# Kernel tuning notes

Hardware: AMD Instinct MI355X
Metric: run time of the kernel (lower is better)

## Reference

```python
import jax, jax.numpy as jnp
import numpy as np

B, S, D = 4, 4096, 1024
DECAY = 0.95


def setup_inputs() -> dict:
    key = jax.random.key(0)
    ks = jax.random.split(key, 7)
    sc = 1.0 / np.sqrt(D)
    return {
        "h": jax.random.normal(ks[0], (B, S, D), jnp.float32),
        "chunk_size": 128,
        "Wq": jax.random.normal(ks[1], (D, D), jnp.float32) * sc,
        "Wk": jax.random.normal(ks[2], (D, D), jnp.float32) * sc,
        "Wv": jax.random.normal(ks[3], (D, D), jnp.float32) * sc,
        "Wo": jax.random.normal(ks[4], (D, D), jnp.float32) * sc,
        "Wg": jax.random.normal(ks[5], (D, D), jnp.float32) * sc,
        "bg": jnp.zeros((D,), jnp.float32),
    }


def reference(h, chunk_size, Wq, Wk, Wv, Wo, Wg, bg):
    bsz, seq_len, d_model = h.shape
    n_chunks = seq_len // chunk_size  # S divisible by chunk_size

    # projections (torch nn.Linear: y = x @ W.T)
    q = jnp.einsum('bsd,ed->bse', h, Wq)
    k = jnp.einsum('bsd,ed->bse', h, Wk)
    v = jnp.einsum('bsd,ed->bse', h, Wv)
    gate = jax.nn.sigmoid(jnp.einsum('bsd,ed->bse', h, Wg) + bg)

    def to_chunks(x):  # [B,S,D] -> [n_chunks, B, T, D]
        return x.reshape(bsz, n_chunks, chunk_size, d_model).transpose(1, 0, 2, 3)

    qc, kc, vc, gc = map(to_chunks, (q, k, v, gate))

    def step(state, inp):
        q_c, k_c, v_c, g_c = inp
        kv = jnp.einsum('btd,bte->bde', k_c, v_c) / chunk_size
        state = DECAY * state + (1.0 - DECAY) * kv
        ret = jnp.einsum('btd,bde->bte', q_c, state)
        return state, ret * g_c

    state0 = jnp.zeros((bsz, d_model, d_model), h.dtype)
    _, out_chunks = jax.lax.scan(step, state0, (qc, kc, vc, gc))
    out = out_chunks.transpose(1, 0, 2, 3).reshape(bsz, seq_len, d_model)
    return jnp.einsum('bsd,ed->bse', out, Wo)
```

## Files before the change

### kernel.cpp

```cpp
#include <hip/hip_runtime.h>
#include <math.h>

#define B_ 4
#define S_ 4096
#define D_ 1024
#define T_ 128
#define NC_ 32
#define DECAY_ 0.95f
#define NPAIR_ 528

typedef __bf16 bf16;
typedef __bf16 bf16x8 __attribute__((ext_vector_type(8)));
typedef __bf16 bf16x4 __attribute__((ext_vector_type(4)));
typedef float f32x4 __attribute__((ext_vector_type(4)));

__device__ __forceinline__ f32x4 mfma16(bf16x8 a, bf16x8 b, f32x4 c) {
  return __builtin_amdgcn_mfma_f32_16x16x32_bf16(a, b, c, 0, 0, 0);
}

__device__ __forceinline__ void gload16(const bf16* g, bf16* l) {
  __builtin_amdgcn_global_load_lds(
      (const __attribute__((address_space(1))) unsigned int*)g,
      (__attribute__((address_space(3))) unsigned int*)l, 16, 0, 0);
}

__global__ void cast_kernel(const float* __restrict__ src, bf16* __restrict__ dst, int n) {
  int i = (blockIdx.x * blockDim.x + threadIdx.x) * 4;
  int stride = gridDim.x * blockDim.x * 4;
  for (; i < n; i += stride) {
    float4 f = *(const float4*)(src + i);
    bf16x4 o = { (bf16)f.x, (bf16)f.y, (bf16)f.z, (bf16)f.w };
    *(bf16x4*)(dst + i) = o;
  }
}

__global__ void wcast_kernel(const float* __restrict__ Wq, const float* __restrict__ Wk,
                             const float* __restrict__ Wv, const float* __restrict__ Wg,
                             const float* __restrict__ Wo,
                             bf16* __restrict__ Wcat, bf16* __restrict__ Wo_bf) {
  const int NW = 1 << 20;
  long gid = ((long)blockIdx.x * blockDim.x + threadIdx.x) * 4;
  int sel = (int)(gid >> 20);
  int off = (int)(gid & (NW - 1));
  const float* src = (sel == 0) ? Wq : (sel == 1) ? Wk : (sel == 2) ? Wv
                   : (sel == 3) ? Wg : Wo;
  bf16* dst = (sel < 4) ? (Wcat + (long)sel * NW) : Wo_bf;
  float4 f = *(const float4*)(src + off);
  bf16x4 o = { (bf16)f.x, (bf16)f.y, (bf16)f.z, (bf16)f.w };
  *(bf16x4*)(dst + off) = o;
}

__global__ __launch_bounds__(256) void gemm_proj(
    const bf16* __restrict__ A, const bf16* __restrict__ W,
    const float* __restrict__ bg,
    bf16* __restrict__ qo, bf16* __restrict__ ko,
    bf16* __restrict__ vT, bf16* __restrict__ go)
{
  __shared__ __align__(16) bf16 As[128 * 64];
  __shared__ __align__(16) bf16 Bs[128 * 64];
  const int K = 1024;
  int m0 = blockIdx.y * 128;
  int n0 = blockIdx.x * 128;
  int tid = threadIdx.x;
  int l = tid & 63, w = tid >> 6;
  int wr = w >> 1, wc = w & 1;
  int wbase = w << 9;

  const bf16* Ab = A + (long)m0 * K;
  const bf16* Wb = W + (long)n0 * K;
  int srow = tid >> 3;
  int scol = (tid & 7) * 8;

  f32x4 acc[4][4] = {};

  for (int k0 = 0; k0 < K; k0 += 64) {
#pragma unroll
    for (int c = 0; c < 4; ++c) {
      gload16(Ab + (long)(c * 32 + srow) * K + k0 + scol, As + c * 2048 + wbase);
      gload16(Wb + (long)(c * 32 + srow) * K + k0 + scol, Bs + c * 2048 + wbase);
    }
    __syncthreads();
#pragma unroll
    for (int ks = 0; ks < 2; ++ks) {
      bf16x8 af[4], bfr[4];
#pragma unroll
      for (int m = 0; m < 4; ++m)
        af[m] = *(const bf16x8*)(As + (wr * 64 + m * 16 + (l & 15)) * 64 + ks * 32 + (l >> 4) * 8);
#pragma unroll
      for (int n = 0; n < 4; ++n)
        bfr[n] = *(const bf16x8*)(Bs + (wc * 64 + n * 16 + (l & 15)) * 64 + ks * 32 + (l >> 4) * 8);
#pragma unroll
      for (int m = 0; m < 4; ++m)
#pragma unroll
        for (int n = 0; n < 4; ++n)
          acc[m][n] = mfma16(af[m], bfr[n], acc[m][n]);
    }
    __syncthreads();
  }

  int widx = n0 >> 10;
  int b = m0 >> 12;
  int chunk = (m0 & 4095) >> 7;

#pragma unroll
  for (int m = 0; m < 4; ++m) {
    int row = wr * 64 + m * 16 + (l >> 4) * 4;
#pragma unroll
    for (int n = 0; n < 4; ++n) {
      int col = (n0 & 1023) + wc * 64 + n * 16 + (l & 15);
      if (widx == 2) {
        bf16x4 pk = { (bf16)acc[m][n][0], (bf16)acc[m][n][1],
                      (bf16)acc[m][n][2], (bf16)acc[m][n][3] };
        *(bf16x4*)(vT + ((long)(b * NC_ + chunk) * D_ + col) * T_ + row) = pk;
      } else if (widx < 2) {
        bf16* dst = (widx == 0) ? qo : ko;
#pragma unroll
        for (int r = 0; r < 4; ++r)
          dst[(long)(m0 + row + r) * D_ + col] = (bf16)acc[m][n][r];
      } else {
        float bgv = bg[col];
#pragma unroll
        for (int r = 0; r < 4; ++r) {
          float x = acc[m][n][r] + bgv;
          go[(long)(m0 + row + r) * D_ + col] = (bf16)(1.0f / (1.0f + __expf(-x)));
        }
      }
    }
  }
}

__global__ __launch_bounds__(256) void qk_kernel(
    const bf16* __restrict__ q, const bf16* __restrict__ k,
    bf16* __restrict__ Plo, bf16* __restrict__ Phi)
{
  __shared__ __align__(16) bf16 As[128 * 32];
  __shared__ __align__(16) bf16 Bs[128 * 32];
  const int K = 1024;
  int p = blockIdx.x, b = blockIdx.y;
  int n = (int)((sqrtf(8.f * (float)p + 1.f) - 1.f) * 0.5f);
  while ((n + 1) * (n + 2) / 2 <= p) ++n;
  while (n * (n + 1) / 2 > p) --n;
  int j = p - n * (n + 1) / 2;

  int tid = threadIdx.x;
  int l = tid & 63, w = tid >> 6;
  int wr = w >> 1, wc = w & 1;
  int wbase = w << 9;

  const bf16* Ab = q + (long)(b * S_ + n * T_) * K;
  const bf16* Wb = k + (long)(b * S_ + j * T_) * K;
  int lrow = tid >> 2, lcol = (tid & 3) * 8;

  f32x4 acc[4][4] = {};

  for (int k0 = 0; k0 < K; k0 += 32) {
    gload16(Ab + (long)lrow * K + k0 + lcol, As + wbase);
    gload16(Ab + (long)(lrow + 64) * K + k0 + lcol, As + 2048 + wbase);
    gload16(Wb + (long)lrow * K + k0 + lcol, Bs + wbase);
    gload16(Wb + (long)(lrow + 64) * K + k0 + lcol, Bs + 2048 + wbase);
    __syncthreads();
    bf16x8 af[4], bfr[4];
#pragma unroll
    for (int m = 0; m < 4; ++m)
      af[m] = *(const bf16x8*)(As + (wr * 64 + m * 16 + (l & 15)) * 32 + (l >> 4) * 8);
#pragma unroll
    for (int nn = 0; nn < 4; ++nn)
      bfr[nn] = *(const bf16x8*)(Bs + (wc * 64 + nn * 16 + (l & 15)) * 32 + (l >> 4) * 8);
#pragma unroll
    for (int m = 0; m < 4; ++m)
#pragma unroll
      for (int nn = 0; nn < 4; ++nn)
        acc[m][nn] = mfma16(af[m], bfr[nn], acc[m][nn]);
    __syncthreads();
  }

  float c = powf(DECAY_, (float)(n - j)) * ((1.0f - DECAY_) / (float)T_);
  int tile = b * NPAIR_ + p;
  bf16* Pt = (tile < 1024) ? (Plo + (long)tile * 16384)
                           : (Phi + (long)(tile - 1024) * 16384);

#pragma unroll
  for (int m = 0; m < 4; ++m) {
    int row = wr * 64 + m * 16 + (l >> 4) * 4;
#pragma unroll
    for (int nn = 0; nn < 4; ++nn) {
      int col = wc * 64 + nn * 16 + (l & 15);
#pragma unroll
      for (int r = 0; r < 4; ++r)
        Pt[(long)(row + r) * T_ + col] = (bf16)(acc[m][nn][r] * c);
    }
  }
}

__global__ __launch_bounds__(256) void pv_kernel(
    const bf16* __restrict__ Plo, const bf16* __restrict__ Phi,
    const bf16* __restrict__ vT, const bf16* __restrict__ g,
    bf16* __restrict__ mid)
{
  __shared__ __align__(16) bf16 As[128 * 32];
  __shared__ __align__(16) bf16 Bs[128 * 32];
  int et = blockIdx.x;
  int n  = 31 - blockIdx.y;
  int b  = blockIdx.z;
  int e0 = et * 128;
  int tid = threadIdx.x, l = tid & 63, w = tid >> 6;
  int wr = w >> 1, wc = w & 1;
  int wbase = w << 9;
  int lrow = tid >> 2, lcol = (tid & 3) * 8;
  int pbase = b * NPAIR_ + n * (n + 1) / 2;

  f32x4 acc[4][4] = {};

  for (int j = 0; j <= n; ++j) {
    int tile = pbase + j;
    const bf16* Pt = (tile < 1024) ? (Plo + (long)tile * 16384)
                                   : (Phi + (long)(tile - 1024) * 16384);
    const bf16* Vt = vT + (long)(b * NC_ + j) * D_ * T_ + (long)e0 * T_;
#pragma unroll
    for (int kk = 0; kk < 4; ++kk) {
      int k0 = kk * 32;
      gload16(Pt + (long)lrow * T_ + k0 + lcol, As + wbase);
      gload16(Pt + (long)(lrow + 64) * T_ + k0 + lcol, As + 2048 + wbase);
      gload16(Vt + (long)lrow * T_ + k0 + lcol, Bs + wbase);
      gload16(Vt + (long)(lrow + 64) * T_ + k0 + lcol, Bs + 2048 + wbase);
      __syncthreads();
      bf16x8 af[4], bv[4];
#pragma unroll
      for (int m = 0; m < 4; ++m)
        af[m] = *(const bf16x8*)(As + (wr * 64 + m * 16 + (l & 15)) * 32 + (l >> 4) * 8);
#pragma unroll
      for (int nn = 0; nn < 4; ++nn)
        bv[nn] = *(const bf16x8*)(Bs + (wc * 64 + nn * 16 + (l & 15)) * 32 + (l >> 4) * 8);
#pragma unroll
      for (int m = 0; m < 4; ++m)
#pragma unroll
        for (int nn = 0; nn < 4; ++nn)
          acc[m][nn] = mfma16(af[m], bv[nn], acc[m][nn]);
      __syncthreads();
    }
  }

#pragma unroll
  for (int m = 0; m < 4; ++m) {
    int trow = n * T_ + wr * 64 + m * 16 + (l >> 4) * 4;
#pragma unroll
    for (int nn = 0; nn < 4; ++nn) {
      int col = e0 + wc * 64 + nn * 16 + (l & 15);
#pragma unroll
      for (int r = 0; r < 4; ++r) {
        long idx = ((long)b * S_ + trow + r) * D_ + col;
        float gv = (float)g[idx];
        mid[idx] = (bf16)(acc[m][nn][r] * gv);
      }
    }
  }
}

__global__ __launch_bounds__(256) void gemm_out(
    const bf16* __restrict__ A, const bf16* __restrict__ W,
    float* __restrict__ C)
{
  __shared__ __align__(16) bf16 As[128 * 32];
  __shared__ __align__(16) bf16 Bs[128 * 32];
  const int K = 1024;
  int m0 = blockIdx.y * 128;
  int n0 = blockIdx.x * 128;
  int tid = threadIdx.x;
  int l = tid & 63, w = tid >> 6;
  int wr = w >> 1, wc = w & 1;
  int wbase = w << 9;

  const bf16* Ab = A + (long)m0 * K;
  const bf16* Wb = W + (long)n0 * K;
  int lrow = tid >> 2, lcol = (tid & 3) * 8;

  f32x4 acc[4][4] = {};

  for (int k0 = 0; k0 < K; k0 += 32) {
    gload16(Ab + (long)lrow * K + k0 + lcol, As + wbase);
    gload16(Ab + (long)(lrow + 64) * K + k0 + lcol, As + 2048 + wbase);
    gload16(Wb + (long)lrow * K + k0 + lcol, Bs + wbase);
    gload16(Wb + (long)(lrow + 64) * K + k0 + lcol, Bs + 2048 + wbase);
    __syncthreads();
    bf16x8 af[4], bfr[4];
#pragma unroll
    for (int m = 0; m < 4; ++m)
      af[m] = *(const bf16x8*)(As + (wr * 64 + m * 16 + (l & 15)) * 32 + (l >> 4) * 8);
#pragma unroll
    for (int n = 0; n < 4; ++n)
      bfr[n] = *(const bf16x8*)(Bs + (wc * 64 + n * 16 + (l & 15)) * 32 + (l >> 4) * 8);
#pragma unroll
    for (int m = 0; m < 4; ++m)
#pragma unroll
      for (int n = 0; n < 4; ++n)
        acc[m][n] = mfma16(af[m], bfr[n], acc[m][n]);
    __syncthreads();
  }

#pragma unroll
  for (int m = 0; m < 4; ++m) {
    int row = m0 + wr * 64 + m * 16 + (l >> 4) * 4;
#pragma unroll
    for (int n = 0; n < 4; ++n) {
      int col = n0 + wc * 64 + n * 16 + (l & 15);
#pragma unroll
      for (int r = 0; r < 4; ++r)
        C[(long)(row + r) * D_ + col] = acc[m][n][r];
    }
  }
}

extern "C" void kernel_launch(void* const* d_in, const int* in_sizes, int n_in,
                              void* d_out, int out_size, void* d_ws, size_t ws_size,
                              hipStream_t stream) {
  const float* h  = (const float*)d_in[0];
  const float* Wq = (const float*)d_in[2];
  const float* Wk = (const float*)d_in[3];
  const float* Wv = (const float*)d_in[4];
  const float* Wo = (const float*)d_in[5];
  const float* Wg = (const float*)d_in[6];
  const float* bg = (const float*)d_in[7];
  float* out = (float*)d_out;

  bf16* ws = (bf16*)d_ws;
  const long NHD = (long)B_ * S_ * D_;
  const long NW  = (long)D_ * D_;

  bf16* h_bf  = ws;  ws += NHD;
  bf16* Wcat  = ws;  ws += 4 * NW;
  bf16* Wo_bf = ws;  ws += NW;
  bf16* q_bf  = ws;  ws += NHD;
  bf16* k_bf  = ws;  ws += NHD;
  bf16* vT    = ws;  ws += NHD;
  bf16* g_bf  = ws;  ws += NHD;
  bf16* P_hi  = ws;  ws += (long)(4 * NPAIR_ - 1024) * 16384;

  bf16* P_lo = h_bf;
  bf16* mid  = q_bf;

  cast_kernel<<<4096, 256, 0, stream>>>(h, h_bf, (int)NHD);
  wcast_kernel<<<5120, 256, 0, stream>>>(Wq, Wk, Wv, Wg, Wo, Wcat, Wo_bf);

  gemm_proj<<<dim3(32, 128), 256, 0, stream>>>(h_bf, Wcat, bg, q_bf, k_bf, vT, g_bf);
  qk_kernel<<<dim3(NPAIR_, 4), 256, 0, stream>>>(q_bf, k_bf, P_lo, P_hi);
  pv_kernel<<<dim3(8, 32, 4), 256, 0, stream>>>(P_lo, P_hi, vT, g_bf, mid);
  gemm_out<<<dim3(8, 128), 256, 0, stream>>>(mid, Wo_bf, out);
}
```

Baseline: 659.4 us.

## Retile projection GEMM to 256x256 with double-buffered swizzled LDS

The projection GEMM moves from 128x128 tiles with 256 threads to 256x256 tiles with 512 threads, giving each wave an 8x4 MFMA fragment grid. LDS loads are double-buffered: a vmcnt-based wait lets the next K tile stream in while the current one computes. Shared memory uses an XOR swizzle to cut bank conflicts on fragment reads. The larger tiles raise per-block data reuse, but occupancy drops to one block per CU and the grid shrinks to 1024 blocks.

New measurement: 599.2 us. -9.1%, faster.

```diff
diff --git a/kernel.cpp b/kernel.cpp
--- a/kernel.cpp
+++ b/kernel.cpp
@@ -50,79 +50,105 @@
   *(bf16x4*)(dst + off) = o;
 }
 
-__global__ __launch_bounds__(256) void gemm_proj(
+__global__ __launch_bounds__(512, 1) void gemm_proj(
     const bf16* __restrict__ A, const bf16* __restrict__ W,
     const float* __restrict__ bg,
     bf16* __restrict__ qo, bf16* __restrict__ ko,
     bf16* __restrict__ vT, bf16* __restrict__ go)
 {
-  __shared__ __align__(16) bf16 As[128 * 64];
-  __shared__ __align__(16) bf16 Bs[128 * 64];
+  __shared__ __align__(16) bf16 As[2][256 * 64];
+  __shared__ __align__(16) bf16 Bs[2][256 * 64];
   const int K = 1024;
-  int m0 = blockIdx.y * 128;
-  int n0 = blockIdx.x * 128;
-  int tid = threadIdx.x;
-  int l = tid & 63, w = tid >> 6;
-  int wr = w >> 1, wc = w & 1;
-  int wbase = w << 9;
+  const int NT = 16;
+  int m0 = blockIdx.y * 256;
+  int n0 = blockIdx.x * 256;
+  int t = threadIdx.x;
+  int l = t & 63, w = t >> 6;
+  int wr = w >> 2, wc = w & 3;
 
   const bf16* Ab = A + (long)m0 * K;
   const bf16* Wb = W + (long)n0 * K;
-  int srow = tid >> 3;
-  int scol = (tid & 7) * 8;
-
-  f32x4 acc[4][4] = {};
-
-  for (int k0 = 0; k0 < K; k0 += 64) {
+
+  int srow_off = t >> 3;
+  int scol_swz = (((t & 7) ^ ((t >> 3) & 7)) * 8);
+  int wdst = w << 9;
+
+  f32x4 acc[8][4] = {};
+
+  auto stage = [&](int buf, int kt) {
 #pragma unroll
     for (int c = 0; c < 4; ++c) {
-      gload16(Ab + (long)(c * 32 + srow) * K + k0 + scol, As + c * 2048 + wbase);
-      gload16(Wb + (long)(c * 32 + srow) * K + k0 + scol, Bs + c * 2048 + wbase);
-    }
-    __syncthreads();
-#pragma unroll
-    for (int ks = 0; ks < 2; ++ks) {
-      bf16x8 af[4], bfr[4];
-#pragma unroll
-      for (int m = 0; m < 4; ++m)
-        af[m] = *(const bf16x8*)(As + (wr * 64 + m * 16 + (l & 15)) * 64 + ks * 32 + (l >> 4) * 8);
-#pragma unroll
-      for (int n = 0; n < 4; ++n)
-        bfr[n] = *(const bf16x8*)(Bs + (wc * 64 + n * 16 + (l & 15)) * 64 + ks * 32 + (l >> 4) * 8);
-#pragma unroll
-      for (int m = 0; m < 4; ++m)
-#pragma unroll
-        for (int n = 0; n < 4; ++n)
-          acc[m][n] = mfma16(af[m], bfr[n], acc[m][n]);
-    }
-    __syncthreads();
+      int r = c * 64 + srow_off;
+      gload16(Ab + (long)r * K + kt * 64 + scol_swz, &As[buf][c * 4096 + wdst]);
+      gload16(Wb + (long)r * K + kt * 64 + scol_swz, &Bs[buf][c * 4096 + wdst]);
+    }
+  };
+
+  auto compute = [&](int buf) {
+    bf16x8 bfrag[4][2];
+#pragma unroll
+    for (int fn = 0; fn < 4; ++fn)
+#pragma unroll
+      for (int ks = 0; ks < 2; ++ks) {
+        int rb = wc * 64 + fn * 16 + (l & 15);
+        int sb = ks * 4 + (l >> 4);
+        bfrag[fn][ks] = *(const bf16x8*)(&Bs[buf][rb * 64 + ((sb ^ (rb & 7)) * 8)]);
+      }
+#pragma unroll
+    for (int fm = 0; fm < 8; ++fm) {
+      int ra = wr * 128 + fm * 16 + (l & 15);
+      int s0 = (l >> 4);
+      bf16x8 a0 = *(const bf16x8*)(&As[buf][ra * 64 + ((s0 ^ (ra & 7)) * 8)]);
+      bf16x8 a1 = *(const bf16x8*)(&As[buf][ra * 64 + (((s0 + 4) ^ (ra & 7)) * 8)]);
+#pragma unroll
+      for (int fn = 0; fn < 4; ++fn) {
+        acc[fm][fn] = mfma16(a0, bfrag[fn][0], acc[fm][fn]);
+        acc[fm][fn] = mfma16(a1, bfrag[fn][1], acc[fm][fn]);
+      }
+    }
+  };
+
+  stage(0, 0);
+  stage(1, 1);
+  for (int kt = 0; kt < NT; ++kt) {
+    if (kt < NT - 1) {
+      asm volatile("s_waitcnt vmcnt(8)" ::: "memory");
+    } else {
+      asm volatile("s_waitcnt vmcnt(0)" ::: "memory");
+    }
+    __builtin_amdgcn_s_barrier();
+    __builtin_amdgcn_sched_barrier(0);
+    compute(kt & 1);
+    __builtin_amdgcn_s_barrier();
+    if (kt + 2 < NT) stage(kt & 1, kt + 2);
   }
 
   int widx = n0 >> 10;
   int b = m0 >> 12;
-  int chunk = (m0 & 4095) >> 7;
-
-#pragma unroll
-  for (int m = 0; m < 4; ++m) {
-    int row = wr * 64 + m * 16 + (l >> 4) * 4;
-#pragma unroll
-    for (int n = 0; n < 4; ++n) {
-      int col = (n0 & 1023) + wc * 64 + n * 16 + (l & 15);
+
+#pragma unroll
+  for (int fm = 0; fm < 8; ++fm) {
+    int rowg = m0 + wr * 128 + fm * 16 + (l >> 4) * 4;
+#pragma unroll
+    for (int fn = 0; fn < 4; ++fn) {
+      int col = (n0 & 1023) + wc * 64 + fn * 16 + (l & 15);
       if (widx == 2) {
-        bf16x4 pk = { (bf16)acc[m][n][0], (bf16)acc[m][n][1],
-                      (bf16)acc[m][n][2], (bf16)acc[m][n][3] };
-        *(bf16x4*)(vT + ((long)(b * NC_ + chunk) * D_ + col) * T_ + row) = pk;
+        int chunk = (rowg & 4095) >> 7;
+        int trow = rowg & 127;
+        bf16x4 pk = { (bf16)acc[fm][fn][0], (bf16)acc[fm][fn][1],
+                      (bf16)acc[fm][fn][2], (bf16)acc[fm][fn][3] };
+        *(bf16x4*)(vT + ((long)(b * NC_ + chunk) * D_ + col) * T_ + trow) = pk;
       } else if (widx < 2) {
         bf16* dst = (widx == 0) ? qo : ko;
 #pragma unroll
         for (int r = 0; r < 4; ++r)
-          dst[(long)(m0 + row + r) * D_ + col] = (bf16)acc[m][n][r];
+          dst[(long)(rowg + r) * D_ + col] = (bf16)acc[fm][fn][r];
       } else {
         float bgv = bg[col];
 #pragma unroll
         for (int r = 0; r < 4; ++r) {
-          float x = acc[m][n][r] + bgv;
-          go[(long)(m0 + row + r) * D_ + col] = (bf16)(1.0f / (1.0f + __expf(-x)));
+          float x = acc[fm][fn][r] + bgv;
+          go[(long)(rowg + r) * D_ + col] = (bf16)(1.0f / (1.0f + __expf(-x)));
         }
       }
     }
@@ -341,7 +367,7 @@
   cast_kernel<<<4096, 256, 0, stream>>>(h, h_bf, (int)NHD);
   wcast_kernel<<<5120, 256, 0, stream>>>(Wq, Wk, Wv, Wg, Wo, Wcat, Wo_bf);
 
-  gemm_proj<<<dim3(32, 128), 256, 0, stream>>>(h_bf, Wcat, bg, q_bf, k_bf, vT, g_bf);
+  gemm_proj<<<dim3(16, 64), 512, 0, stream>>>(h_bf, Wcat, bg, q_bf, k_bf, vT, g_bf);
   qk_kernel<<<dim3(NPAIR_, 4), 256, 0, stream>>>(q_bf, k_bf, P_lo, P_hi);
   pv_kernel<<<dim3(8, 32, 4), 256, 0, stream>>>(P_lo, P_hi, vT, g_bf, mid);
   gemm_out<<<dim3(8, 128), 256, 0, stream>>>(mid, Wo_bf, out);
```
